# Kernel tuning notes

Measured on AMD Instinct MI355X. Metric: run time of the kernel, lower is better.

## Reference

```python
import jax, jax.numpy as jnp
import numpy as np

B, KD, VD = 65536, 512, 512

def setup_inputs() -> dict:
    key = jax.random.key(0)
    ks = jax.random.split(key, 5)
    return {
        "k": jax.random.normal(ks[0], (B, KD), jnp.float32),
        "v": jax.random.normal(ks[1], (B, VD), jnp.float32),
        "W": jax.random.normal(ks[2], (VD, KD), jnp.float32) * 0.02,  # memory.weight
        "S": jax.random.normal(ks[3], (VD, KD), jnp.float32) * 0.01,  # momentum buffer
        "gate_w": jax.random.normal(ks[4], (3, KD), jnp.float32) * 0.02,
        "gate_b": jnp.full((3,), 0.5, jnp.float32),  # nn.init.constant_(bias, 0.5)
    }

def reference(k, v, W, S, gate_w, gate_b):
    sg = jax.lax.stop_gradient
    # memory lookup: Linear(key_dim -> val_dim), no bias
    retrieved = k @ W.T                           # (B, VD)
    diff = retrieved - sg(v)
    loss_memory = jnp.mean(diff * diff)
    # --- TTT update (training path; all detached from autodiff in torch) ---
    # autograd.grad of mse(memory(k), v) w.r.t. W is analytically an outer product:
    # grad = 2/(B*VD) * (k @ W.T - v).T @ k
    d = sg(diff)                                  # loss_ttt uses detached k, v -> same residual values
    grad = (2.0 / (B * VD)) * (d.T @ sg(k))       # (VD, KD)
    # gates from batch-mean key
    gates = jax.nn.sigmoid(gate_w @ sg(jnp.mean(k, axis=0)) + gate_b)  # (3,)
    alpha, eta, theta = gates[0], gates[1], gates[2]
    new_S = eta * sg(S) - theta * grad            # momentum decay + gradient step
    new_W = (1.0 - alpha) * sg(W) + new_S         # gated weight decay + momentum write
    return retrieved, loss_memory, new_W, new_S
```

## Files before the change

### kernel.cpp

```cpp
#include <hip/hip_runtime.h>
#include <hip/hip_bf16.h>

typedef __attribute__((ext_vector_type(8))) short bf16x8;
typedef __attribute__((ext_vector_type(4))) float f32x4;
typedef unsigned int u32;
typedef unsigned short u16;

#define NB 65536
#define NKD 512
#define NVD 512

#define WS_COLSUM 262144
#define WS_LOSS   262656
#define WS_DIFFT_BYTES 1056768

#define OUT_LOSS 33554432
#define OUT_W    33554433
#define OUT_S    33816577

__device__ inline u32 pkbf2(float a, float b) {
    __hip_bfloat162 h2 = __float22bfloat162_rn(make_float2(a, b));
    u32 r;
    __builtin_memcpy(&r, &h2, 4);
    return r;
}

__device__ inline void async16(const u16* g, u16* l) {
    __builtin_amdgcn_global_load_lds(
        (const __attribute__((address_space(1))) u32*)g,
        (__attribute__((address_space(3))) u32*)l, 16, 0, 0);
}

#define PA 72
#define PT 136

__global__ __launch_bounds__(256, 2)
void k1_gemm1(const float* __restrict__ kmat, const float* __restrict__ vmat,
              const float* __restrict__ Wmat, float* __restrict__ out,
              float* __restrict__ ws, u16* __restrict__ diffT) {
    __shared__ u16 sm[18432];
    __shared__ float lred[4];

    const int tid = threadIdx.x;
    const int bx = blockIdx.x;
    const int rowtile = bx >> 2, ntile = bx & 3;
    const long b0 = (long)rowtile * 128;
    const int vd0 = ntile * 128;
    const int wv = tid >> 6, lane = tid & 63;
    const int wm = wv & 1, wn = wv >> 1;
    const int col = lane & 15, kg = lane >> 4;

    const int srow = tid >> 4;
    const int scol = (tid & 15) * 4;

    f32x4 acc[4][4] = {};

    for (int it = 0; it < 8; ++it) {
        __syncthreads();
        const float* gA = kmat + (b0 + srow) * 512 + it * 64 + scol;
        const float* gB = Wmat + (long)(vd0 + srow) * 512 + it * 64 + scol;
#pragma unroll
        for (int i = 0; i < 8; ++i) {
            float4 a = *(const float4*)(gA + (long)i * 16 * 512);
            float4 b = *(const float4*)(gB + (long)i * 16 * 512);
            int r = i * 16 + srow;
            *(uint2*)&sm[r * PA + scol] = make_uint2(pkbf2(a.x, a.y), pkbf2(a.z, a.w));
            *(uint2*)&sm[9216 + r * PA + scol] = make_uint2(pkbf2(b.x, b.y), pkbf2(b.z, b.w));
        }
        __syncthreads();
#pragma unroll
        for (int kk = 0; kk < 2; ++kk) {
            bf16x8 af[4], bfr[4];
#pragma unroll
            for (int i = 0; i < 4; ++i)
                af[i] = *(const bf16x8*)&sm[(wm * 64 + i * 16 + col) * PA + kk * 32 + kg * 8];
#pragma unroll
            for (int j = 0; j < 4; ++j)
                bfr[j] = *(const bf16x8*)&sm[9216 + (wn * 64 + j * 16 + col) * PA + kk * 32 + kg * 8];
#pragma unroll
            for (int i = 0; i < 4; ++i)
#pragma unroll
                for (int j = 0; j < 4; ++j)
                    acc[i][j] = __builtin_amdgcn_mfma_f32_16x16x32_bf16(af[i], bfr[j], acc[i][j], 0, 0, 0);
        }
    }

    __syncthreads();
    u16* smT = sm;

    float lossp = 0.f;
    const int rg = lane >> 4;
#pragma unroll
    for (int i = 0; i < 4; ++i) {
#pragma unroll
        for (int j = 0; j < 4; ++j) {
            int r0 = wm * 64 + i * 16 + rg * 4;
            int c  = wn * 64 + j * 16 + col;
            long gb = b0 + r0;
            float dd[4];
#pragma unroll
            for (int r = 0; r < 4; ++r) {
                float rv = acc[i][j][r];
                long gidx = (gb + r) * 512 + vd0 + c;
                out[gidx] = rv;
                float dv = rv - vmat[gidx];
                lossp += dv * dv;
                dd[r] = dv;
            }
            *(u32*)&smT[c * PT + r0]     = pkbf2(dd[0], dd[1]);
            *(u32*)&smT[c * PT + r0 + 2] = pkbf2(dd[2], dd[3]);
        }
    }

#pragma unroll
    for (int m = 32; m; m >>= 1) lossp += __shfl_xor(lossp, m);
    if (lane == 0) lred[wv] = lossp;
    __syncthreads();
    if (tid == 0) atomicAdd(&ws[WS_LOSS], lred[0] + lred[1] + lred[2] + lred[3]);

    {
        const int c = tid >> 1, h = tid & 1;
        const u16* src = &smT[c * PT + h * 64];
        u16* dst = diffT + ((long)(vd0 + c) << 16) + b0 + h * 64;
#pragma unroll
        for (int q = 0; q < 8; ++q) {
            uint4 t4 = *(const uint4*)(src + q * 8);
            *(uint4*)(dst + q * 8) = t4;
        }
    }
}

__global__ __launch_bounds__(256, 2)
void k2_grad(const u16* __restrict__ diffT, const float* __restrict__ kmat,
             float* __restrict__ ws) {
    __shared__ u16 sm[17408];
    u16* As = sm;
    u16* Bs = sm + 8192;

    const int tid = threadIdx.x;
    const int bx = blockIdx.x;
    const int tile = bx & 15, chunk = bx >> 4;
    const int vd0 = (tile >> 2) * 128, kd0 = (tile & 3) * 128;
    const long b0 = (long)chunk * 2048;
    const int wv = tid >> 6, lane = tid & 63;
    const int wm = wv & 1, wn = wv >> 1;
    const int col = lane & 15, kg = lane >> 4;

    const int bcol = (tid & 63) * 2;
    const int bq = wv * 16;

    f32x4 acc[4][4] = {};
    float cs0 = 0.f, cs1 = 0.f;

    for (int it = 0; it < 32; ++it) {
        __syncthreads();
        {
            const u16* gbase = diffT + ((long)vd0 << 16) + b0 + it * 64;
#pragma unroll
            for (int q = 0; q < 4; ++q) {
                int rowb = wv * 32 + q * 8;
                const u16* g = gbase + ((long)(rowb + (lane >> 3)) << 16) + (lane & 7) * 8;
                async16(g, &As[rowb * 64]);
            }
        }
        {
            const float* gk = kmat + (b0 + it * 64 + bq) * 512 + kd0 + bcol;
            float2 r[16];
#pragma unroll
            for (int i = 0; i < 16; ++i) r[i] = *(const float2*)(gk + (long)i * 512);
#pragma unroll
            for (int i = 0; i < 16; ++i) { cs0 += r[i].x; cs1 += r[i].y; }
            u32 p0[8], p1[8];
#pragma unroll
            for (int i = 0; i < 8; ++i) {
                p0[i] = pkbf2(r[2 * i].x, r[2 * i + 1].x);
                p1[i] = pkbf2(r[2 * i].y, r[2 * i + 1].y);
            }
            *(uint4*)&Bs[bcol * PA + bq]           = make_uint4(p0[0], p0[1], p0[2], p0[3]);
            *(uint4*)&Bs[bcol * PA + bq + 8]       = make_uint4(p0[4], p0[5], p0[6], p0[7]);
            *(uint4*)&Bs[(bcol + 1) * PA + bq]     = make_uint4(p1[0], p1[1], p1[2], p1[3]);
            *(uint4*)&Bs[(bcol + 1) * PA + bq + 8] = make_uint4(p1[4], p1[5], p1[6], p1[7]);
        }
        __syncthreads();
#pragma unroll
        for (int kk = 0; kk < 2; ++kk) {
            bf16x8 af[4], bfr[4];
#pragma unroll
            for (int i = 0; i < 4; ++i)
                af[i] = *(const bf16x8*)&As[(wm * 64 + i * 16 + col) * 64 + kk * 32 + kg * 8];
#pragma unroll
            for (int j = 0; j < 4; ++j)
                bfr[j] = *(const bf16x8*)&Bs[(wn * 64 + j * 16 + col) * PA + kk * 32 + kg * 8];
#pragma unroll
            for (int i = 0; i < 4; ++i)
#pragma unroll
                for (int j = 0; j < 4; ++j)
                    acc[i][j] = __builtin_amdgcn_mfma_f32_16x16x32_bf16(af[i], bfr[j], acc[i][j], 0, 0, 0);
        }
    }

    const int rg = lane >> 4;
#pragma unroll
    for (int i = 0; i < 4; ++i)
#pragma unroll
        for (int j = 0; j < 4; ++j)
#pragma unroll
            for (int r = 0; r < 4; ++r) {
                int vd = vd0 + wm * 64 + i * 16 + rg * 4 + r;
                int kd = kd0 + wn * 64 + j * 16 + col;
                atomicAdd(&ws[vd * 512 + kd], acc[i][j][r]);
            }

    if (vd0 == 0) {
        __syncthreads();
        float* cred = (float*)sm;
        cred[bcol * 4 + wv] = cs0;
        cred[(bcol + 1) * 4 + wv] = cs1;
        __syncthreads();
        if (tid < 128) {
            float s = cred[tid * 4] + cred[tid * 4 + 1] + cred[tid * 4 + 2] + cred[tid * 4 + 3];
            atomicAdd(&ws[WS_COLSUM + kd0 + tid], s);
        }
    }
}

__global__ __launch_bounds__(256)
void k3_final(const float* __restrict__ Wmat, const float* __restrict__ Smat,
              const float* __restrict__ gw, const float* __restrict__ gb,
              const float* __restrict__ ws, float* __restrict__ out) {
    __shared__ float gates[3];
    const int tid = threadIdx.x;
    if (tid < 64) {
        float d0 = 0.f, d1 = 0.f, d2 = 0.f;
#pragma unroll
        for (int i = 0; i < 8; ++i) {
            int kd = i * 64 + tid;
            float km = ws[WS_COLSUM + kd] * (1.0f / 65536.0f);
            d0 += gw[kd] * km;
            d1 += gw[512 + kd] * km;
            d2 += gw[1024 + kd] * km;
        }
#pragma unroll
        for (int m = 32; m; m >>= 1) {
            d0 += __shfl_xor(d0, m);
            d1 += __shfl_xor(d1, m);
            d2 += __shfl_xor(d2, m);
        }
        if (tid == 0) {
            gates[0] = 1.f / (1.f + __expf(-(d0 + gb[0])));
            gates[1] = 1.f / (1.f + __expf(-(d1 + gb[1])));
            gates[2] = 1.f / (1.f + __expf(-(d2 + gb[2])));
        }
    }
    __syncthreads();
    const float alpha = gates[0], eta = gates[1], theta = gates[2];
    const int i = blockIdx.x * 256 + tid;
    float g = ws[i] * 5.9604644775390625e-8f;
    float ns = eta * Smat[i] - theta * g;
    out[OUT_S + i] = ns;
    out[OUT_W + i] = (1.f - alpha) * Wmat[i] + ns;
    if (blockIdx.x == 0 && tid == 0)
        out[OUT_LOSS] = ws[WS_LOSS] * 2.98023223876953125e-8f;
}

extern "C" void kernel_launch(void* const* d_in, const int* in_sizes, int n_in,
                              void* d_out, int out_size, void* d_ws, size_t ws_size,
                              hipStream_t stream) {
    const float* k  = (const float*)d_in[0];
    const float* v  = (const float*)d_in[1];
    const float* W  = (const float*)d_in[2];
    const float* S  = (const float*)d_in[3];
    const float* gw = (const float*)d_in[4];
    const float* gb = (const float*)d_in[5];
    float* out = (float*)d_out;
    float* ws  = (float*)d_ws;
    u16* diffT = (u16*)((char*)d_ws + WS_DIFFT_BYTES);

    hipMemsetAsync(d_ws, 0, (WS_LOSS + 1) * sizeof(float), stream);

    hipLaunchKernelGGL(k1_gemm1, dim3(2048), dim3(256), 0, stream, k, v, W, out, ws, diffT);
    hipLaunchKernelGGL(k2_grad,  dim3(512),  dim3(256), 0, stream, diffT, k, ws);
    hipLaunchKernelGGL(k3_final, dim3(1024), dim3(256), 0, stream, W, S, gw, gb, ws, out);
}
```

Measured before the change: 567.0 us.

## Double-buffer shared memory and prefetch next tile in both GEMM kernels

Both the forward GEMM and the gradient GEMM now use two LDS buffers and load the next K-slice from global memory into registers (or via async LDS loads) while MFMA work runs on the current slice. This removes one barrier per iteration and is meant to hide global load latency behind compute. It doubles LDS usage per block and raises register pressure from the held prefetch registers, which could reduce occupancy.

```diff
diff --git a/kernel.cpp b/kernel.cpp
--- a/kernel.cpp
+++ b/kernel.cpp
@@ -38,7 +38,7 @@
 void k1_gemm1(const float* __restrict__ kmat, const float* __restrict__ vmat,
               const float* __restrict__ Wmat, float* __restrict__ out,
               float* __restrict__ ws, u16* __restrict__ diffT) {
-    __shared__ u16 sm[18432];
+    __shared__ u16 sm[36864];
     __shared__ float lred[4];
 
     const int tid = threadIdx.x;
@@ -55,28 +55,43 @@
 
     f32x4 acc[4][4] = {};
 
+    const float* gA = kmat + (b0 + srow) * 512 + scol;
+    const float* gB = Wmat + (long)(vd0 + srow) * 512 + scol;
+
+    float4 ra[8], rb[8];
+#pragma unroll
+    for (int i = 0; i < 8; ++i) {
+        ra[i] = *(const float4*)(gA + (long)i * 16 * 512);
+        rb[i] = *(const float4*)(gB + (long)i * 16 * 512);
+    }
+
     for (int it = 0; it < 8; ++it) {
+        u16* Ab = sm + (it & 1) * 18432;
+        u16* Bb = Ab + 9216;
+#pragma unroll
+        for (int i = 0; i < 8; ++i) {
+            int r = i * 16 + srow;
+            *(uint2*)&Ab[r * PA + scol] = make_uint2(pkbf2(ra[i].x, ra[i].y), pkbf2(ra[i].z, ra[i].w));
+            *(uint2*)&Bb[r * PA + scol] = make_uint2(pkbf2(rb[i].x, rb[i].y), pkbf2(rb[i].z, rb[i].w));
+        }
         __syncthreads();
-        const float* gA = kmat + (b0 + srow) * 512 + it * 64 + scol;
-        const float* gB = Wmat + (long)(vd0 + srow) * 512 + it * 64 + scol;
-#pragma unroll
-        for (int i = 0; i < 8; ++i) {
-            float4 a = *(const float4*)(gA + (long)i * 16 * 512);
-            float4 b = *(const float4*)(gB + (long)i * 16 * 512);
-            int r = i * 16 + srow;
-            *(uint2*)&sm[r * PA + scol] = make_uint2(pkbf2(a.x, a.y), pkbf2(a.z, a.w));
-            *(uint2*)&sm[9216 + r * PA + scol] = make_uint2(pkbf2(b.x, b.y), pkbf2(b.z, b.w));
-        }
-        __syncthreads();
+        if (it < 7) {
+            gA += 64; gB += 64;
+#pragma unroll
+            for (int i = 0; i < 8; ++i) {
+                ra[i] = *(const float4*)(gA + (long)i * 16 * 512);
+                rb[i] = *(const float4*)(gB + (long)i * 16 * 512);
+            }
+        }
 #pragma unroll
         for (int kk = 0; kk < 2; ++kk) {
             bf16x8 af[4], bfr[4];
 #pragma unroll
             for (int i = 0; i < 4; ++i)
-                af[i] = *(const bf16x8*)&sm[(wm * 64 + i * 16 + col) * PA + kk * 32 + kg * 8];
+                af[i] = *(const bf16x8*)&Ab[(wm * 64 + i * 16 + col) * PA + kk * 32 + kg * 8];
 #pragma unroll
             for (int j = 0; j < 4; ++j)
-                bfr[j] = *(const bf16x8*)&sm[9216 + (wn * 64 + j * 16 + col) * PA + kk * 32 + kg * 8];
+                bfr[j] = *(const bf16x8*)&Bb[(wn * 64 + j * 16 + col) * PA + kk * 32 + kg * 8];
 #pragma unroll
             for (int i = 0; i < 4; ++i)
 #pragma unroll
@@ -133,9 +148,7 @@
 __global__ __launch_bounds__(256, 2)
 void k2_grad(const u16* __restrict__ diffT, const float* __restrict__ kmat,
              float* __restrict__ ws) {
-    __shared__ u16 sm[17408];
-    u16* As = sm;
-    u16* Bs = sm + 8192;
+    __shared__ u16 sm[34816];
 
     const int tid = threadIdx.x;
     const int bx = blockIdx.x;
@@ -152,29 +165,28 @@
     f32x4 acc[4][4] = {};
     float cs0 = 0.f, cs1 = 0.f;
 
+    const int rowb0 = wv * 32;
+    const u16* gAit = diffT + ((long)(vd0 + rowb0 + (lane >> 3)) << 16) + b0 + (lane & 7) * 8;
+    const float* gk0 = kmat + (b0 + bq) * 512 + kd0 + bcol;
+
+    float2 rB[16];
+#pragma unroll
+    for (int q = 0; q < 4; ++q)
+        async16(gAit + ((long)(q * 8) << 16), &sm[(rowb0 + q * 8) * 64]);
+#pragma unroll
+    for (int i = 0; i < 16; ++i) rB[i] = *(const float2*)(gk0 + (long)i * 512);
+
     for (int it = 0; it < 32; ++it) {
-        __syncthreads();
+        u16* As = sm + (it & 1) * 17408;
+        u16* Bs = As + 8192;
         {
-            const u16* gbase = diffT + ((long)vd0 << 16) + b0 + it * 64;
-#pragma unroll
-            for (int q = 0; q < 4; ++q) {
-                int rowb = wv * 32 + q * 8;
-                const u16* g = gbase + ((long)(rowb + (lane >> 3)) << 16) + (lane & 7) * 8;
-                async16(g, &As[rowb * 64]);
-            }
-        }
-        {
-            const float* gk = kmat + (b0 + it * 64 + bq) * 512 + kd0 + bcol;
-            float2 r[16];
-#pragma unroll
-            for (int i = 0; i < 16; ++i) r[i] = *(const float2*)(gk + (long)i * 512);
-#pragma unroll
-            for (int i = 0; i < 16; ++i) { cs0 += r[i].x; cs1 += r[i].y; }
+#pragma unroll
+            for (int i = 0; i < 16; ++i) { cs0 += rB[i].x; cs1 += rB[i].y; }
             u32 p0[8], p1[8];
 #pragma unroll
             for (int i = 0; i < 8; ++i) {
-                p0[i] = pkbf2(r[2 * i].x, r[2 * i + 1].x);
-                p1[i] = pkbf2(r[2 * i].y, r[2 * i + 1].y);
+                p0[i] = pkbf2(rB[2 * i].x, rB[2 * i + 1].x);
+                p1[i] = pkbf2(rB[2 * i].y, rB[2 * i + 1].y);
             }
             *(uint4*)&Bs[bcol * PA + bq]           = make_uint4(p0[0], p0[1], p0[2], p0[3]);
             *(uint4*)&Bs[bcol * PA + bq + 8]       = make_uint4(p0[4], p0[5], p0[6], p0[7]);
@@ -182,6 +194,16 @@
             *(uint4*)&Bs[(bcol + 1) * PA + bq + 8] = make_uint4(p1[4], p1[5], p1[6], p1[7]);
         }
         __syncthreads();
+        if (it < 31) {
+            u16* An = sm + (((it & 1) ^ 1)) * 17408;
+            const u16* gan = gAit + (it + 1) * 64;
+#pragma unroll
+            for (int q = 0; q < 4; ++q)
+                async16(gan + ((long)(q * 8) << 16), &An[(rowb0 + q * 8) * 64]);
+            const float* gkn = gk0 + (long)(it + 1) * 64 * 512;
+#pragma unroll
+            for (int i = 0; i < 16; ++i) rB[i] = *(const float2*)(gkn + (long)i * 512);
+        }
 #pragma unroll
         for (int kk = 0; kk < 2; ++kk) {
             bf16x8 af[4], bfr[4];
```

After: 496.8 us. 1.14x faster.
